# Kernel optimization log

Hardware: AMD Instinct MI355X
Metric: run time of the kernel (lower is better)

The kernel has to match this reference:

```python
import jax, jax.numpy as jnp
from jax import lax
import numpy as np

RADIUS = 0.05
N_SEEDS = 40

def _farthest_point_sample(xyz, npoint):
    # xyz: [B, N, 3] -> seed indices [B, npoint]
    B, N, _ = xyz.shape
    dist0 = jnp.full((B, N), 1e10, dtype=xyz.dtype)
    far0 = jnp.zeros((B,), dtype=jnp.int32)  # deterministic init (torch uses randint)
    batch_idx = jnp.arange(B)

    def step(carry, _):
        distance, farthest = carry
        centroid = xyz[batch_idx, farthest][:, None, :]          # [B,1,3]
        d = jnp.sum((xyz - centroid) ** 2, axis=-1)              # [B,N]
        distance = jnp.minimum(distance, d)
        new_far = jnp.argmax(distance, axis=-1).astype(jnp.int32)
        return (distance, new_far), farthest

    _, cents = lax.scan(step, (dist0, far0), None, length=npoint)
    return cents.T                                               # [B, npoint]

def setup_inputs() -> dict:
    key = jax.random.key(0)
    pcs = jax.random.uniform(key, (16, 65536, 3), dtype=jnp.float32)
    return {"pcs": pcs}

def reference(pcs) -> jnp.ndarray:
    B, N, C = pcs.shape
    S = N_SEEDS
    seeds = _farthest_point_sample(pcs, S)                       # [B,S] int
    new_xyz = pcs[jnp.arange(B)[:, None], seeds]                 # [B,S,3]
    # squared pairwise distances seeds->points: [B,S,N]
    sqrdists = (jnp.sum(new_xyz ** 2, -1)[:, :, None]
                + jnp.sum(pcs ** 2, -1)[:, None, :]
                - 2.0 * jnp.einsum('bsc,bnc->bsn', new_xyz, pcs))
    relu_dists = jax.nn.relu(RADIUS ** 2 - sqrdists)
    den_mat = jnp.sum(relu_dists, axis=2)                        # [B,S]
    den_var = jnp.var(den_mat, axis=1, ddof=1).mean()            # torch.var is unbiased
    return den_var
```

## Files before the change

kernel.cpp:

```cpp
#include <hip/hip_runtime.h>

typedef unsigned long long ull;

#define NB    16
#define NPTS  65536
#define NSEED 40
#define BPB   16
#define TPB   1024
#define NW    16
#define PPT   4
#define R2    0.0025f
#define PAYLOAD 0xFFFFFFFFFFFFull
#define DONEG 40ull

__device__ __forceinline__ ull packdi(float v, int idx) {
  return ((ull)__float_as_uint(v) << 16) | (ull)((unsigned)(idx ^ 0xFFFF) & 0xFFFFu);
}

__global__ __launch_bounds__(TPB, 4) void fps_den_kernel(
    const float* __restrict__ pcs, ull* __restrict__ slots,
    ull* __restrict__ pden, float* __restrict__ out)
{
  const int beta = blockIdx.x >> 4;
  const int blk  = blockIdx.x & 15;
  const int tid  = threadIdx.x;
  const int lane = tid & 63;
  const int wav  = tid >> 6;
  const float* __restrict__ base = pcs + (size_t)beta * (NPTS * 3);

  __shared__ ull   sRedP[2][NW];
  __shared__ float sWx[2], sWy[2], sWz[2];
  __shared__ float sW0x[4 * 64], sW0y[4 * 64], sW0z[4 * 64];
  __shared__ float sDen[NW][NSEED];
  __shared__ float sV[NB];

  float px[PPT], py[PPT], pz[PPT], dist[PPT];
#pragma unroll
  for (int j = 0; j < PPT; ++j) {
    int n = blk * (TPB * PPT) + j * TPB + tid;
    px[j] = base[n * 3 + 0];
    py[j] = base[n * 3 + 1];
    pz[j] = base[n * 3 + 2];
    dist[j] = 1e10f;
  }

  if (wav == 0) {
#pragma unroll
    for (int j = 0; j < PPT; ++j) {
      sW0x[j * 64 + lane] = px[j];
      sW0y[j * 64 + lane] = py[j];
      sW0z[j * 64 + lane] = pz[j];
    }
  }

  float cx = base[0], cy = base[1], cz = base[2];

  ull* myslots = slots + (size_t)beta * (2 * BPB);
  ull* mypden  = pden + ((size_t)beta * BPB + blk) * NSEED;

  for (int k = 0; k < NSEED - 1; ++k) {
    ull bestp = 0;
#pragma unroll
    for (int j = 0; j < PPT; ++j) {
      float dx = px[j] - cx, dy = py[j] - cy, dz = pz[j] - cz;
      float d  = __fadd_rn(__fadd_rn(__fmul_rn(dx, dx), __fmul_rn(dy, dy)),
                           __fmul_rn(dz, dz));
      float nd = fminf(dist[j], d);
      dist[j]  = nd;
      int n    = blk * (TPB * PPT) + j * TPB + tid;
      ull p    = packdi(nd, n);
      if (p > bestp) bestp = p;
    }
    ull mx = bestp;
#pragma unroll
    for (int o = 32; o > 0; o >>= 1) {
      ull q = __shfl_xor(mx, o, 64);
      mx = mx > q ? mx : q;
    }
    if (lane == 0) sRedP[k & 1][wav] = mx;
    __syncthreads();

    const ull gen = (ull)(k + 1);
    const ull g48 = gen << 48;
    ull* arr = myslots + (size_t)((k + 1) & 1) * BPB;

    if (wav == 0) {
      ull rp = (lane < NW) ? sRedP[k & 1][lane] : 0;
      ull m2 = rp;
#pragma unroll
      for (int o = 8; o > 0; o >>= 1) {
        ull q = __shfl_xor(m2, o, 64);
        m2 = m2 > q ? m2 : q;
      }
      if (lane == 0)
        __hip_atomic_store(&arr[blk], g48 | (m2 & PAYLOAD),
                           __ATOMIC_RELAXED, __HIP_MEMORY_SCOPE_AGENT);

      ull  key = 0;
      bool got = (lane >= NW);
      ull* ap = &arr[lane & 15];
      ull t0 = 0, t1 = 0;
      if (lane < NW) {
        t0 = __hip_atomic_load(ap, __ATOMIC_RELAXED, __HIP_MEMORY_SCOPE_AGENT);
        t1 = __hip_atomic_load(ap, __ATOMIC_RELAXED, __HIP_MEMORY_SCOPE_AGENT);
      }
      for (;;) {
        if (!got && (t0 >> 48) == gen) { key = t0 & PAYLOAD; got = true; }
        if (__all((int)got)) break;
        t0 = t1;
        if (!got)
          t1 = __hip_atomic_load(ap, __ATOMIC_RELAXED, __HIP_MEMORY_SCOPE_AGENT);
      }

      ull m = key;
#pragma unroll
      for (int o = 32; o > 0; o >>= 1) {
        ull q = __shfl_xor(m, o, 64);
        m = m > q ? m : q;
      }
      int widx = (int)((unsigned)((m ^ 0xFFFFull) & 0xFFFFull));
      widx = __builtin_amdgcn_readfirstlane(widx);
      const float* q = base + 3 * (size_t)widx;
      float wx2 = q[0], wy2 = q[1], wz2 = q[2];
      if (lane == 0) {
        sWx[k & 1] = wx2; sWy[k & 1] = wy2; sWz[k & 1] = wz2;
      }
    } else {
      float da = 0.f;
#pragma unroll
      for (int j = 0; j < PPT; ++j) {
        float dx = px[j] - cx, dy = py[j] - cy, dz = pz[j] - cz;
        float d  = dx * dx + dy * dy + dz * dz;
        da += fmaxf(R2 - d, 0.f);
      }
#pragma unroll
      for (int o = 32; o > 0; o >>= 1) da += __shfl_xor(da, o, 64);
      if (lane == 0) sDen[wav][k] = da;

      if (wav == 1) {
        float a0 = 0.f;
#pragma unroll
        for (int j = 0; j < PPT; ++j) {
          float dx = sW0x[j * 64 + lane] - cx;
          float dy = sW0y[j * 64 + lane] - cy;
          float dz = sW0z[j * 64 + lane] - cz;
          float d  = dx * dx + dy * dy + dz * dz;
          a0 += fmaxf(R2 - d, 0.f);
        }
#pragma unroll
        for (int o = 32; o > 0; o >>= 1) a0 += __shfl_xor(a0, o, 64);
        if (lane == 0) sDen[0][k] = a0;
      }

      if (wav == 15 && lane == 0 && k > 0) {
        float t = 0.f;
#pragma unroll
        for (int w = 0; w < NW; ++w) t += sDen[w][k - 1];
        __hip_atomic_store(&mypden[k - 1],
                           (DONEG << 48) | (ull)__float_as_uint(t),
                           __ATOMIC_RELAXED, __HIP_MEMORY_SCOPE_AGENT);
      }
    }
    __syncthreads();
    cx = sWx[k & 1]; cy = sWy[k & 1]; cz = sWz[k & 1];
  }

  if (wav >= 1) {
    float a = 0.f;
#pragma unroll
    for (int j = 0; j < PPT; ++j) {
      float dx = px[j] - cx, dy = py[j] - cy, dz = pz[j] - cz;
      float d  = dx * dx + dy * dy + dz * dz;
      a += fmaxf(R2 - d, 0.f);
    }
#pragma unroll
    for (int o = 32; o > 0; o >>= 1) a += __shfl_xor(a, o, 64);
    if (lane == 0) sDen[wav][NSEED - 1] = a;

    if (wav == 1) {
      float a0 = 0.f;
#pragma unroll
      for (int j = 0; j < PPT; ++j) {
        float dx = sW0x[j * 64 + lane] - cx;
        float dy = sW0y[j * 64 + lane] - cy;
        float dz = sW0z[j * 64 + lane] - cz;
        float d  = dx * dx + dy * dy + dz * dz;
        a0 += fmaxf(R2 - d, 0.f);
      }
#pragma unroll
      for (int o = 32; o > 0; o >>= 1) a0 += __shfl_xor(a0, o, 64);
      if (lane == 0) sDen[0][NSEED - 1] = a0;
    }
  }
  __syncthreads();

  if (tid < 2) {
    int s = (NSEED - 2) + tid;
    float t = 0.f;
#pragma unroll
    for (int w = 0; w < NW; ++w) t += sDen[w][s];
    __hip_atomic_store(&mypden[s], (DONEG << 48) | (ull)__float_as_uint(t),
                       __ATOMIC_RELAXED, __HIP_MEMORY_SCOPE_AGENT);
  }

  if (blockIdx.x == 0) {
    __syncthreads();
    if (tid < NB * NSEED) {
      int b0 = tid / NSEED, s = tid - b0 * NSEED;
      float a = 0.f;
#pragma unroll
      for (int c = 0; c < 2; ++c) {
        ull v[8];
#pragma unroll
        for (int b = 0; b < 8; ++b)
          v[b] = __hip_atomic_load(
              &pden[((size_t)b0 * BPB + c * 8 + b) * NSEED + s],
              __ATOMIC_RELAXED, __HIP_MEMORY_SCOPE_AGENT);
        for (;;) {
          bool ok = true;
#pragma unroll
          for (int b = 0; b < 8; ++b)
            if ((v[b] >> 48) != DONEG) {
              ok = false;
              v[b] = __hip_atomic_load(
                  &pden[((size_t)b0 * BPB + c * 8 + b) * NSEED + s],
                  __ATOMIC_RELAXED, __HIP_MEMORY_SCOPE_AGENT);
            }
          if (ok) break;
        }
#pragma unroll
        for (int b = 0; b < 8; ++b)
          a += __uint_as_float((unsigned)(v[b] & 0xFFFFFFFFull));
      }
      sDen[b0][s] = a;
    }
    __syncthreads();
    if (tid < NB) {
      float m = 0.f;
      for (int s = 0; s < NSEED; ++s) m += sDen[tid][s];
      m /= (float)NSEED;
      float q = 0.f;
      for (int s = 0; s < NSEED; ++s) { float d = sDen[tid][s] - m; q += d * d; }
      sV[tid] = q / (float)(NSEED - 1);
    }
    __syncthreads();
    if (tid == 0) {
      float v = 0.f;
      for (int i = 0; i < NB; ++i) v += sV[i];
      out[0] = v / (float)NB;
    }
  }
}

extern "C" void kernel_launch(void* const* d_in, const int* in_sizes, int n_in,
                              void* d_out, int out_size, void* d_ws, size_t ws_size,
                              hipStream_t stream) {
  const float* pcs = (const float*)d_in[0];
  float* out  = (float*)d_out;
  ull*   pden = (ull*)d_ws;
  ull*   slots = (ull*)((char*)d_ws + 81920);
  fps_den_kernel<<<dim3(NB * BPB), dim3(TPB), 0, stream>>>(pcs, slots, pden, out);
}
```

Measured before the change: 162.3 us.

## Carry winner coordinates through reductions and slots instead of reloading from global

Each thread, wave and block now carries the xyz coordinates of its current farthest point alongside the packed max key. The coordinates are packed into two extra 48-bit slot records per block, so wave 0 reads the winning centroid directly from the exchange slots. This removes the dependent global load of the winner's coordinates on the serial critical path of each FPS iteration. In exchange it adds ballot and shuffle work, three times as many slot stores and polls per iteration, and a larger workspace footprint for the slots.

```diff
diff --git a/kernel.cpp b/kernel.cpp
--- a/kernel.cpp
+++ b/kernel.cpp
@@ -29,6 +29,7 @@
   const float* __restrict__ base = pcs + (size_t)beta * (NPTS * 3);
 
   __shared__ ull   sRedP[2][NW];
+  __shared__ float sRedX[2][NW], sRedY[2][NW], sRedZ[2][NW];
   __shared__ float sWx[2], sWy[2], sWz[2];
   __shared__ float sW0x[4 * 64], sW0y[4 * 64], sW0z[4 * 64];
   __shared__ float sDen[NW][NSEED];
@@ -55,11 +56,11 @@
 
   float cx = base[0], cy = base[1], cz = base[2];
 
-  ull* myslots = slots + (size_t)beta * (2 * BPB);
+  ull* myslots = slots + (size_t)beta * (2 * 3 * BPB);
   ull* mypden  = pden + ((size_t)beta * BPB + blk) * NSEED;
 
   for (int k = 0; k < NSEED - 1; ++k) {
-    ull bestp = 0;
+    ull bestp = 0; float bx = 0.f, by = 0.f, bz = 0.f;
 #pragma unroll
     for (int j = 0; j < PPT; ++j) {
       float dx = px[j] - cx, dy = py[j] - cy, dz = pz[j] - cz;
@@ -69,7 +70,7 @@
       dist[j]  = nd;
       int n    = blk * (TPB * PPT) + j * TPB + tid;
       ull p    = packdi(nd, n);
-      if (p > bestp) bestp = p;
+      if (p > bestp) { bestp = p; bx = px[j]; by = py[j]; bz = pz[j]; }
     }
     ull mx = bestp;
 #pragma unroll
@@ -77,12 +78,20 @@
       ull q = __shfl_xor(mx, o, 64);
       mx = mx > q ? mx : q;
     }
-    if (lane == 0) sRedP[k & 1][wav] = mx;
+    ull bal = __ballot(bestp == mx);
+    int src = __ffsll((long long)bal) - 1;
+    float gx = __shfl(bx, src, 64);
+    float gy = __shfl(by, src, 64);
+    float gz = __shfl(bz, src, 64);
+    if (lane == 0) {
+      sRedP[k & 1][wav] = mx;
+      sRedX[k & 1][wav] = gx; sRedY[k & 1][wav] = gy; sRedZ[k & 1][wav] = gz;
+    }
     __syncthreads();
 
     const ull gen = (ull)(k + 1);
     const ull g48 = gen << 48;
-    ull* arr = myslots + (size_t)((k + 1) & 1) * BPB;
+    ull* arr = myslots + (size_t)((k + 1) & 1) * (3 * BPB);
 
     if (wav == 0) {
       ull rp = (lane < NW) ? sRedP[k & 1][lane] : 0;
@@ -92,38 +101,52 @@
         ull q = __shfl_xor(m2, o, 64);
         m2 = m2 > q ? m2 : q;
       }
-      if (lane == 0)
-        __hip_atomic_store(&arr[blk], g48 | (m2 & PAYLOAD),
+      ull bal2 = __ballot((rp == m2) && (lane < NW));
+      int s2 = __ffsll((long long)bal2) - 1;
+      unsigned xb = __float_as_uint(sRedX[k & 1][s2]);
+      unsigned yb = __float_as_uint(sRedY[k & 1][s2]);
+      unsigned zb = __float_as_uint(sRedZ[k & 1][s2]);
+      ull rec = g48 | (m2 & PAYLOAD);
+      if (lane == 1) rec = g48 | ((ull)xb << 16) | (ull)(yb >> 16);
+      if (lane == 2) rec = g48 | ((ull)(yb & 0xFFFFu) << 32) | (ull)zb;
+      if (lane < 3)
+        __hip_atomic_store(&arr[lane * NW + blk], rec,
                            __ATOMIC_RELAXED, __HIP_MEMORY_SCOPE_AGENT);
 
-      ull  key = 0;
-      bool got = (lane >= NW);
-      ull* ap = &arr[lane & 15];
+      ull  pay = 0;
+      bool got = (lane >= 3 * NW);
+      ull* ap = &arr[lane];
       ull t0 = 0, t1 = 0;
-      if (lane < NW) {
+      if (!got) {
         t0 = __hip_atomic_load(ap, __ATOMIC_RELAXED, __HIP_MEMORY_SCOPE_AGENT);
         t1 = __hip_atomic_load(ap, __ATOMIC_RELAXED, __HIP_MEMORY_SCOPE_AGENT);
       }
       for (;;) {
-        if (!got && (t0 >> 48) == gen) { key = t0 & PAYLOAD; got = true; }
+        if (!got && (t0 >> 48) == gen) { pay = t0 & PAYLOAD; got = true; }
         if (__all((int)got)) break;
         t0 = t1;
         if (!got)
           t1 = __hip_atomic_load(ap, __ATOMIC_RELAXED, __HIP_MEMORY_SCOPE_AGENT);
       }
 
-      ull m = key;
+      ull pl = (lane < NW) ? pay : 0;
+      ull m = pl;
 #pragma unroll
       for (int o = 32; o > 0; o >>= 1) {
         ull q = __shfl_xor(m, o, 64);
         m = m > q ? m : q;
       }
-      int widx = (int)((unsigned)((m ^ 0xFFFFull) & 0xFFFFull));
-      widx = __builtin_amdgcn_readfirstlane(widx);
-      const float* q = base + 3 * (size_t)widx;
-      float wx2 = q[0], wy2 = q[1], wz2 = q[2];
+      ull balw = __ballot((pl == m) && (lane < NW));
+      int srcw = __ffsll((long long)balw) - 1;
+      ull f1 = __shfl(pay, NW + srcw, 64);
+      ull f2 = __shfl(pay, 2 * NW + srcw, 64);
       if (lane == 0) {
-        sWx[k & 1] = wx2; sWy[k & 1] = wy2; sWz[k & 1] = wz2;
+        unsigned xb2 = (unsigned)(f1 >> 16);
+        unsigned yb2 = (unsigned)(((f1 & 0xFFFFull) << 16) | ((f2 >> 32) & 0xFFFFull));
+        unsigned zb2 = (unsigned)(f2 & 0xFFFFFFFFull);
+        sWx[k & 1] = __uint_as_float(xb2);
+        sWy[k & 1] = __uint_as_float(yb2);
+        sWz[k & 1] = __uint_as_float(zb2);
       }
     } else {
       float da = 0.f;
```

Measured after the change: 166.2 us. 2.4% more time.
